# Kernel optimization log

Measured on AMD Instinct MI355X. Metric: run time of the kernel, lower is better.

Reference implementation:

```python
import jax, jax.numpy as jnp
import numpy as np

N_WINDOW = 128  # |i-j| < N_WINDOW kept
D_K = 64

def setup_inputs() -> dict:
    key = jax.random.key(0)
    kq, kk, kv = jax.random.split(key, 3)
    B, H, S, D = 2, 8, 2048, D_K
    Q = jax.random.normal(kq, (B, H, S, D), dtype=jnp.float32)
    K = jax.random.normal(kk, (B, H, S, D), dtype=jnp.float32)
    V = jax.random.normal(kv, (B, H, S, D), dtype=jnp.float32)
    return {"Q": Q, "K": K, "V": V}

def reference(Q, K, V):
    S = Q.shape[-2]
    # scores: [B, H, S, S]
    scores = jnp.einsum('bhqd,bhkd->bhqk', Q, K) / jnp.sqrt(jnp.float32(D_K))
    idx = jnp.arange(S)
    band = jnp.abs(idx[:, None] - idx[None, :]) < N_WINDOW  # [S, S] band mask
    scores = jnp.where(band[None, None, :, :], scores, -jnp.inf)
    attn = jax.nn.softmax(scores, axis=-1)
    context = jnp.einsum('bhqk,bhkd->bhqd', attn, V)
    return (context, attn)
```

## Files before the change

kernel.cpp:

```cpp
#include <hip/hip_runtime.h>
#include <math.h>

#define S_LEN 2048
#define DK 64
#define TQ 32
#define KLW 320
#define CH 64
#define NCH 5
#define PSTR 324
#define PSTR4 81
#define KSTR 72
#define KSTR4 18

typedef __attribute__((ext_vector_type(8))) short bf16x8;
typedef __attribute__((ext_vector_type(4))) float f32x4;
typedef __attribute__((ext_vector_type(4))) short short4v;

__device__ __forceinline__ short f2bf(float f) {
    unsigned u = __float_as_uint(f);
    unsigned r = (u + 0x7fffu + ((u >> 16) & 1u)) >> 16;
    return (short)r;
}

__global__ __launch_bounds__(256, 2) void band_attn_mfma(
    const float* __restrict__ Q,
    const float* __restrict__ K,
    const float* __restrict__ V,
    float* __restrict__ ctx_out,
    float* __restrict__ attn_out)
{
    __shared__ __align__(16) float Ps[TQ * PSTR];
    __shared__ __align__(16) short Qs[TQ * KSTR];
    __shared__ __align__(16) short St[CH * KSTR];

    const int tid  = threadIdx.x;
    const int bh   = blockIdx.x >> 6;
    const int q0   = (blockIdx.x & 63) * TQ;
    const int base = q0 - 128;

    const int lane = tid & 63;
    const int wv   = tid >> 6;
    const int col  = lane & 15;
    const int quad = lane >> 4;

    const float4* Qg = (const float4*)(Q + ((size_t)bh * S_LEN + q0) * DK);
    const float4* Kg = (const float4*)(K + (size_t)bh * S_LEN * DK);
    const float4* Vg = (const float4*)(V + (size_t)bh * S_LEN * DK);

    {
        short4v* Qs4 = (short4v*)Qs;
        #pragma unroll
        for (int h = 0; h < 2; ++h) {
            int idx = tid + h * 256;
            int r = idx >> 4, c4 = idx & 15;
            float4 v = Qg[r * 16 + c4];
            short4v s = { f2bf(v.x * 0.125f), f2bf(v.y * 0.125f),
                          f2bf(v.z * 0.125f), f2bf(v.w * 0.125f) };
            Qs4[r * KSTR4 + c4] = s;
        }
    }

    for (int c = 0; c < NCH; ++c) {
        __syncthreads();
        {
            short4v* St4 = (short4v*)St;
            #pragma unroll
            for (int h = 0; h < 4; ++h) {
                int idx = tid + h * 256;
                int r = idx >> 4, c4 = idx & 15;
                int kg = base + c * CH + r;
                float4 v = {0.f, 0.f, 0.f, 0.f};
                if ((unsigned)kg < S_LEN) v = Kg[(size_t)kg * 16 + c4];
                short4v s = { f2bf(v.x), f2bf(v.y), f2bf(v.z), f2bf(v.w) };
                St4[r * KSTR4 + c4] = s;
            }
        }
        __syncthreads();

        const int kl = c * CH + 16 * wv + col;
        const int kg = base + kl;
        #pragma unroll
        for (int qt = 0; qt < 2; ++qt) {
            f32x4 acc = {0.f, 0.f, 0.f, 0.f};
            #pragma unroll
            for (int h = 0; h < 2; ++h) {
                bf16x8 a = *(const bf16x8*)(Qs + (16 * qt + col) * KSTR + h * 32 + quad * 8);
                bf16x8 b = *(const bf16x8*)(St + (16 * wv + col) * KSTR + h * 32 + quad * 8);
                acc = __builtin_amdgcn_mfma_f32_16x16x32_bf16(a, b, acc, 0, 0, 0);
            }
            #pragma unroll
            for (int r = 0; r < 4; ++r) {
                int qloc = 16 * qt + quad * 4 + r;
                bool ok = ((unsigned)kg < S_LEN) && (kl > qloc) && (kl <= qloc + 255);
                Ps[qloc * PSTR + kl] = ok ? acc[r] : -INFINITY;
            }
        }
    }
    __syncthreads();

    #pragma unroll
    for (int rr = 0; rr < 8; ++rr) {
        float* row = Ps + (wv * 8 + rr) * PSTR;
        float v[5];
        #pragma unroll
        for (int j = 0; j < 5; ++j) v[j] = row[lane + 64 * j];
        float m = fmaxf(fmaxf(fmaxf(v[0], v[1]), fmaxf(v[2], v[3])), v[4]);
        #pragma unroll
        for (int off = 32; off > 0; off >>= 1) m = fmaxf(m, __shfl_xor(m, off, 64));
        float e[5], sum = 0.f;
        #pragma unroll
        for (int j = 0; j < 5; ++j) { e[j] = __expf(v[j] - m); sum += e[j]; }
        #pragma unroll
        for (int off = 32; off > 0; off >>= 1) sum += __shfl_xor(sum, off, 64);
        const float inv = 1.0f / sum;
        #pragma unroll
        for (int j = 0; j < 5; ++j) row[lane + 64 * j] = e[j] * inv;
    }

    f32x4 o0 = {0.f, 0.f, 0.f, 0.f}, o1 = {0.f, 0.f, 0.f, 0.f};
    for (int c = 0; c < NCH; ++c) {
        __syncthreads();
        {
            #pragma unroll
            for (int h = 0; h < 4; ++h) {
                int idx = tid + h * 256;
                int r = idx >> 4, c4 = idx & 15;
                int kg = base + c * CH + r;
                float4 v = {0.f, 0.f, 0.f, 0.f};
                if ((unsigned)kg < S_LEN) v = Vg[(size_t)kg * 16 + c4];
                St[(4 * c4 + 0) * KSTR + r] = f2bf(v.x);
                St[(4 * c4 + 1) * KSTR + r] = f2bf(v.y);
                St[(4 * c4 + 2) * KSTR + r] = f2bf(v.z);
                St[(4 * c4 + 3) * KSTR + r] = f2bf(v.w);
            }
        }
        __syncthreads();

        #pragma unroll
        for (int h = 0; h < 2; ++h) {
            bf16x8 b = *(const bf16x8*)(St + (16 * wv + col) * KSTR + h * 32 + quad * 8);
            #pragma unroll
            for (int qt = 0; qt < 2; ++qt) {
                const float* pp = Ps + (16 * qt + col) * PSTR + c * CH + h * 32 + quad * 8;
                f32x4 p0 = *(const f32x4*)(pp);
                f32x4 p1 = *(const f32x4*)(pp + 4);
                bf16x8 a = { f2bf(p0[0]), f2bf(p0[1]), f2bf(p0[2]), f2bf(p0[3]),
                             f2bf(p1[0]), f2bf(p1[1]), f2bf(p1[2]), f2bf(p1[3]) };
                if (qt == 0) o0 = __builtin_amdgcn_mfma_f32_16x16x32_bf16(a, b, o0, 0, 0, 0);
                else         o1 = __builtin_amdgcn_mfma_f32_16x16x32_bf16(a, b, o1, 0, 0, 0);
            }
        }
    }

    {
        float* Cg = ctx_out + ((size_t)bh * S_LEN + q0) * DK;
        #pragma unroll
        for (int r = 0; r < 4; ++r) {
            Cg[(size_t)(quad * 4 + r) * DK + 16 * wv + col]        = o0[r];
            Cg[(size_t)(16 + quad * 4 + r) * DK + 16 * wv + col]   = o1[r];
        }
    }

    {
        f32x4* A4 = (f32x4*)(attn_out + ((size_t)bh * S_LEN + q0) * S_LEN);
        const f32x4* Ps4 = (const f32x4*)Ps;
        const int b0 = 4 * tid - base;
        const int b1 = b0 + 1024;
        const f32x4 z = {0.f, 0.f, 0.f, 0.f};
        for (int r = 0; r < TQ; ++r) {
            f32x4 va = ((unsigned)b0 < KLW) ? Ps4[r * PSTR4 + (b0 >> 2)] : z;
            f32x4 vb = ((unsigned)b1 < KLW) ? Ps4[r * PSTR4 + (b1 >> 2)] : z;
            A4[(size_t)r * 512 + tid]       = va;
            A4[(size_t)r * 512 + tid + 256] = vb;
        }
    }
}

extern "C" void kernel_launch(void* const* d_in, const int* in_sizes, int n_in,
                              void* d_out, int out_size, void* d_ws, size_t ws_size,
                              hipStream_t stream) {
    const float* Q = (const float*)d_in[0];
    const float* K = (const float*)d_in[1];
    const float* V = (const float*)d_in[2];
    float* out = (float*)d_out;

    const int BH = in_sizes[0] / (S_LEN * DK);
    const size_t ctx_elems = (size_t)BH * S_LEN * DK;
    float* ctx  = out;
    float* attn = out + ctx_elems;

    dim3 grid(BH * (S_LEN / TQ));
    band_attn_mfma<<<grid, 256, 0, stream>>>(Q, K, V, ctx, attn);
}
```

Measured before the change: 326.4 us.

## Load Q/K/V MFMA fragments directly from global memory, dropping LDS staging

Removes the shared-memory staging buffers for Q, K and V. Each lane now loads its MFMA operand fragments straight from global memory into registers and converts them to bf16 there, which eliminates most __syncthreads calls and the LDS transpose of V. Launch bounds rise to 3 blocks per SM because LDS use drops, and the attention write-out is reorganised so each wave writes its own 8 rows. The cost is uncoalesced strided scalar loads for V and redundant global reads of K and V across waves, which now depend on the cache.

```diff
diff --git a/kernel.cpp b/kernel.cpp
--- a/kernel.cpp
+++ b/kernel.cpp
@@ -5,16 +5,12 @@
 #define DK 64
 #define TQ 32
 #define KLW 320
-#define CH 64
 #define NCH 5
 #define PSTR 324
 #define PSTR4 81
-#define KSTR 72
-#define KSTR4 18
 
 typedef __attribute__((ext_vector_type(8))) short bf16x8;
 typedef __attribute__((ext_vector_type(4))) float f32x4;
-typedef __attribute__((ext_vector_type(4))) short short4v;
 
 __device__ __forceinline__ short f2bf(float f) {
     unsigned u = __float_as_uint(f);
@@ -22,7 +18,14 @@
     return (short)r;
 }
 
-__global__ __launch_bounds__(256, 2) void band_attn_mfma(
+__device__ __forceinline__ bf16x8 pack8(f32x4 a, f32x4 b) {
+    bf16x8 r;
+    r[0] = f2bf(a[0]); r[1] = f2bf(a[1]); r[2] = f2bf(a[2]); r[3] = f2bf(a[3]);
+    r[4] = f2bf(b[0]); r[5] = f2bf(b[1]); r[6] = f2bf(b[2]); r[7] = f2bf(b[3]);
+    return r;
+}
+
+__global__ __launch_bounds__(256, 3) void band_attn_v4(
     const float* __restrict__ Q,
     const float* __restrict__ K,
     const float* __restrict__ V,
@@ -30,8 +33,6 @@
     float* __restrict__ attn_out)
 {
     __shared__ __align__(16) float Ps[TQ * PSTR];
-    __shared__ __align__(16) short Qs[TQ * KSTR];
-    __shared__ __align__(16) short St[CH * KSTR];
 
     const int tid  = threadIdx.x;
     const int bh   = blockIdx.x >> 6;
@@ -43,55 +44,42 @@
     const int col  = lane & 15;
     const int quad = lane >> 4;
 
-    const float4* Qg = (const float4*)(Q + ((size_t)bh * S_LEN + q0) * DK);
-    const float4* Kg = (const float4*)(K + (size_t)bh * S_LEN * DK);
-    const float4* Vg = (const float4*)(V + (size_t)bh * S_LEN * DK);
+    const float* Qh = Q + ((size_t)bh * S_LEN + q0) * DK;
+    const float* Kh = K + (size_t)bh * S_LEN * DK;
+    const float* Vh = V + (size_t)bh * S_LEN * DK;
 
-    {
-        short4v* Qs4 = (short4v*)Qs;
+    bf16x8 qf[2][2];
+    #pragma unroll
+    for (int qt = 0; qt < 2; ++qt)
         #pragma unroll
         for (int h = 0; h < 2; ++h) {
-            int idx = tid + h * 256;
-            int r = idx >> 4, c4 = idx & 15;
-            float4 v = Qg[r * 16 + c4];
-            short4v s = { f2bf(v.x * 0.125f), f2bf(v.y * 0.125f),
-                          f2bf(v.z * 0.125f), f2bf(v.w * 0.125f) };
-            Qs4[r * KSTR4 + c4] = s;
+            const float* qp = Qh + (size_t)(16 * qt + col) * DK + 32 * h + 8 * quad;
+            f32x4 a = *(const f32x4*)qp;
+            f32x4 b = *(const f32x4*)(qp + 4);
+            a *= 0.125f; b *= 0.125f;
+            qf[qt][h] = pack8(a, b);
         }
-    }
 
+    #pragma unroll
     for (int c = 0; c < NCH; ++c) {
-        __syncthreads();
-        {
-            short4v* St4 = (short4v*)St;
-            #pragma unroll
-            for (int h = 0; h < 4; ++h) {
-                int idx = tid + h * 256;
-                int r = idx >> 4, c4 = idx & 15;
-                int kg = base + c * CH + r;
-                float4 v = {0.f, 0.f, 0.f, 0.f};
-                if ((unsigned)kg < S_LEN) v = Kg[(size_t)kg * 16 + c4];
-                short4v s = { f2bf(v.x), f2bf(v.y), f2bf(v.z), f2bf(v.w) };
-                St4[r * KSTR4 + c4] = s;
-            }
+        const int kl  = c * 64 + 16 * wv + col;
+        const int kg  = base + kl;
+        const int kgc = min(max(kg, 0), S_LEN - 1);
+        bf16x8 kf[2];
+        #pragma unroll
+        for (int h = 0; h < 2; ++h) {
+            const float* kp = Kh + (size_t)kgc * DK + 32 * h + 8 * quad;
+            kf[h] = pack8(*(const f32x4*)kp, *(const f32x4*)(kp + 4));
         }
-        __syncthreads();
-
-        const int kl = c * CH + 16 * wv + col;
-        const int kg = base + kl;
         #pragma unroll
         for (int qt = 0; qt < 2; ++qt) {
             f32x4 acc = {0.f, 0.f, 0.f, 0.f};
-            #pragma unroll
-            for (int h = 0; h < 2; ++h) {
-                bf16x8 a = *(const bf16x8*)(Qs + (16 * qt + col) * KSTR + h * 32 + quad * 8);
-                bf16x8 b = *(const bf16x8*)(St + (16 * wv + col) * KSTR + h * 32 + quad * 8);
-                acc = __builtin_amdgcn_mfma_f32_16x16x32_bf16(a, b, acc, 0, 0, 0);
-            }
+            acc = __builtin_amdgcn_mfma_f32_16x16x32_bf16(qf[qt][0], kf[0], acc, 0, 0, 0);
+            acc = __builtin_amdgcn_mfma_f32_16x16x32_bf16(qf[qt][1], kf[1], acc, 0, 0, 0);
             #pragma unroll
             for (int r = 0; r < 4; ++r) {
-                int qloc = 16 * qt + quad * 4 + r;
-                bool ok = ((unsigned)kg < S_LEN) && (kl > qloc) && (kl <= qloc + 255);
+                const int qloc = 16 * qt + quad * 4 + r;
+                const bool ok = ((unsigned)kg < S_LEN) && (kl > qloc) && (kl <= qloc + 255);
                 Ps[qloc * PSTR + kl] = ok ? acc[r] : -INFINITY;
             }
         }
@@ -116,38 +104,33 @@
         #pragma unroll
         for (int j = 0; j < 5; ++j) row[lane + 64 * j] = e[j] * inv;
     }
+    __syncthreads();
 
     f32x4 o0 = {0.f, 0.f, 0.f, 0.f}, o1 = {0.f, 0.f, 0.f, 0.f};
+    const float* vcol = Vh + 16 * wv + col;
+    #pragma unroll
     for (int c = 0; c < NCH; ++c) {
-        __syncthreads();
-        {
-            #pragma unroll
-            for (int h = 0; h < 4; ++h) {
-                int idx = tid + h * 256;
-                int r = idx >> 4, c4 = idx & 15;
-                int kg = base + c * CH + r;
-                float4 v = {0.f, 0.f, 0.f, 0.f};
-                if ((unsigned)kg < S_LEN) v = Vg[(size_t)kg * 16 + c4];
-                St[(4 * c4 + 0) * KSTR + r] = f2bf(v.x);
-                St[(4 * c4 + 1) * KSTR + r] = f2bf(v.y);
-                St[(4 * c4 + 2) * KSTR + r] = f2bf(v.z);
-                St[(4 * c4 + 3) * KSTR + r] = f2bf(v.w);
-            }
-        }
-        __syncthreads();
-
         #pragma unroll
         for (int h = 0; h < 2; ++h) {
-            bf16x8 b = *(const bf16x8*)(St + (16 * wv + col) * KSTR + h * 32 + quad * 8);
+            const int k0 = base + c * 64 + 32 * h + 8 * quad;
+            f32x4 va, vb;
+            #pragma unroll
+            for (int j = 0; j < 4; ++j) {
+                int kgc = min(max(k0 + j, 0), S_LEN - 1);
+                va[j] = vcol[(size_t)kgc * DK];
+            }
+            #pragma unroll
+            for (int j = 0; j < 4; ++j) {
+                int kgc = min(max(k0 + 4 + j, 0), S_LEN - 1);
+                vb[j] = vcol[(size_t)kgc * DK];
+            }
+            bf16x8 vf = pack8(va, vb);
             #pragma unroll
             for (int qt = 0; qt < 2; ++qt) {
-                const float* pp = Ps + (16 * qt + col) * PSTR + c * CH + h * 32 + quad * 8;
-                f32x4 p0 = *(const f32x4*)(pp);
-                f32x4 p1 = *(const f32x4*)(pp + 4);
-                bf16x8 a = { f2bf(p0[0]), f2bf(p0[1]), f2bf(p0[2]), f2bf(p0[3]),
-                             f2bf(p1[0]), f2bf(p1[1]), f2bf(p1[2]), f2bf(p1[3]) };
-                if (qt == 0) o0 = __builtin_amdgcn_mfma_f32_16x16x32_bf16(a, b, o0, 0, 0, 0);
-                else         o1 = __builtin_amdgcn_mfma_f32_16x16x32_bf16(a, b, o1, 0, 0, 0);
+                const float* pp = Ps + (size_t)(16 * qt + col) * PSTR + c * 64 + 32 * h + 8 * quad;
+                bf16x8 pf = pack8(*(const f32x4*)pp, *(const f32x4*)(pp + 4));
+                if (qt == 0) o0 = __builtin_amdgcn_mfma_f32_16x16x32_bf16(pf, vf, o0, 0, 0, 0);
+                else         o1 = __builtin_amdgcn_mfma_f32_16x16x32_bf16(pf, vf, o1, 0, 0, 0);
             }
         }
     }
@@ -156,22 +139,24 @@
         float* Cg = ctx_out + ((size_t)bh * S_LEN + q0) * DK;
         #pragma unroll
         for (int r = 0; r < 4; ++r) {
-            Cg[(size_t)(quad * 4 + r) * DK + 16 * wv + col]        = o0[r];
-            Cg[(size_t)(16 + quad * 4 + r) * DK + 16 * wv + col]   = o1[r];
+            Cg[(size_t)(quad * 4 + r) * DK + 16 * wv + col]      = o0[r];
+            Cg[(size_t)(16 + quad * 4 + r) * DK + 16 * wv + col] = o1[r];
         }
     }
 
     {
-        f32x4* A4 = (f32x4*)(attn_out + ((size_t)bh * S_LEN + q0) * S_LEN);
+        const int kloff4 = (q0 >> 2) - 32;
+        f32x4* A4 = (f32x4*)(attn_out + ((size_t)bh * S_LEN + q0 + 8 * wv) * S_LEN);
         const f32x4* Ps4 = (const f32x4*)Ps;
-        const int b0 = 4 * tid - base;
-        const int b1 = b0 + 1024;
         const f32x4 z = {0.f, 0.f, 0.f, 0.f};
-        for (int r = 0; r < TQ; ++r) {
-            f32x4 va = ((unsigned)b0 < KLW) ? Ps4[r * PSTR4 + (b0 >> 2)] : z;
-            f32x4 vb = ((unsigned)b1 < KLW) ? Ps4[r * PSTR4 + (b1 >> 2)] : z;
-            A4[(size_t)r * 512 + tid]       = va;
-            A4[(size_t)r * 512 + tid + 256] = vb;
+        #pragma unroll 8
+        for (int i = 0; i < 64; ++i) {
+            const int idx  = i * 64 + lane;
+            const int r    = idx >> 9;
+            const int slot = idx & 511;
+            const int kl4  = slot - kloff4;
+            f32x4 v = ((unsigned)kl4 < 80u) ? Ps4[(8 * wv + r) * PSTR4 + kl4] : z;
+            A4[(size_t)r * 512 + slot] = v;
         }
     }
 }
@@ -190,5 +175,5 @@
     float* attn = out + ctx_elems;
 
     dim3 grid(BH * (S_LEN / TQ));
-    band_attn_mfma<<<grid, 256, 0, stream>>>(Q, K, V, ctx, attn);
+    band_attn_v4<<<grid, 256, 0, stream>>>(Q, K, V, ctx, attn);
 }
```

Result: faster. 303.8 us (-6.9%).
